# Optimization experiments

Hardware: AMD Instinct MI355X
Metric: run time of the kernel (lower is better)

## Reference

```python
import jax, jax.numpy as jnp
import numpy as np

TR = 14.7e-3
NT = 144
TAU = 1.8
T0 = TAU
T1B = 1.65
FA_PARAMS = (3.0, 12.0)
B = 262144


def _build_buffers():
    # t = arange(Nt)*TR + t0
    t = np.arange(NT, dtype=np.float64) * TR + T0
    # QUADRATIC flip-angle schedule: all t >= t0, so N = Nt
    n = NT
    alpha = FA_PARAMS[0] + (FA_PARAMS[1] - FA_PARAMS[0]) * (np.arange(n) / (n - 1)) ** 2
    # Attenuation recursion: R[0]=1, R[i]=R[i-1]*cos(deg2rad(alpha[i-1])) for t[i]>t0
    R = np.concatenate([[1.0], np.cumprod(np.cos(np.deg2rad(alpha[:-1])))])
    return (t.astype(np.float32), alpha.astype(np.float32), R.astype(np.float32))


def setup_inputs() -> dict:
    key = jax.random.key(0)
    x = jax.random.uniform(key, (B, 4), dtype=jnp.float32)  # [delta_t, s, p, amp]
    t, alpha, R = _build_buffers()
    return {"x": x, "t": jnp.asarray(t), "alpha": jnp.asarray(alpha), "R": jnp.asarray(R)}


def _togammainc(X, A):
    # scipy clamps negatives to 0 in both args, then regularized lower incomplete gamma P(A, X)
    X = jnp.maximum(X, 0.0)
    A = jnp.broadcast_to(jnp.maximum(A, 0.0), X.shape)
    return jax.scipy.special.gammainc(A, X)


def reference(x, t, alpha, R):
    delta_t = x[:, 0:1]  # [B,1]
    s = x[:, 1:2]
    p = x[:, 2:3]
    amp = x[:, 3:4]

    a = 1.0 + p * s                     # [B,1]
    sprime = s + 1.0 / T1B              # [B,1]
    SF = 2.0 * jnp.exp(-delta_t / T1B) * (s / sprime) ** a  # [B,1]

    td = t[None, :] - delta_t           # [B,Nt]
    G = _togammainc(sprime * td, a) - _togammainc(sprime * (td - TAU), a)  # [B,Nt]
    E = jnp.sin(jnp.deg2rad(alpha))     # [Nt]

    S = SF * R[None, :] * G * E[None, :]  # [B,Nt]
    return amp * S
```

## Files before the change

kernel.cpp:

```cpp
#include <hip/hip_runtime.h>
#include <cmath>

#define NT 144

typedef float v2f __attribute__((ext_vector_type(2)));


__global__ __launch_bounds__(256) void dynangio_kernel(
    const float* __restrict__ x,
    const float* __restrict__ t,
    const float* __restrict__ alpha,
    const float* __restrict__ R,
    float* __restrict__ out,
    int B)
{
    __shared__ alignas(16) float sh_t[NT];
    __shared__ alignas(16) float sh_re[NT];
    const int tid = threadIdx.x;
    if (tid < NT) {
        sh_t[tid]  = t[tid];
        sh_re[tid] = R[tid] * sinf(alpha[tid] * 0.017453292519943295f);
    }
    __syncthreads();

    const int c   = tid & 3;
    const int row = blockIdx.x * 64 + (tid >> 2);
    if (row >= B) return;

    const float4 xi = reinterpret_cast<const float4*>(x)[row];
    const float dt  = xi.x;
    const float s   = xi.y;
    const float p   = xi.z;
    const float amp = xi.w;

    const float T1B   = 1.65f;
    const float TAU   = 1.8f;
    const float LOG2E = 1.4426950408889634f;

    const float u  = p * s;
    const float a  = 1.0f + u;
    const float sp = s + (1.0f / T1B);

    float g = 0.035868343f;
    g = g * u - 0.193527818f;
    g = g * u + 0.482199394f;
    g = g * u - 0.756704078f;
    g = g * u + 0.918206857f;
    g = g * u - 0.897056937f;
    g = g * u + 0.988205891f;
    g = g * u - 0.577191652f;
    g = g * u + 1.0f;
    const float Ga1 = (1.0f + u) * g;

    const float d18 = a + 18.0f;
    const float d17 = (a + 17.0f) * d18;
    const float d16 = (a + 16.0f) * d17;
    const float d15 = (a + 15.0f) * d16;
    const float d14 = (a + 14.0f) * d15;
    const float d13 = (a + 13.0f) * d14;
    const float d12 = (a + 12.0f) * d13;
    const float d11 = (a + 11.0f) * d12;
    const float d10 = (a + 10.0f) * d11;
    const float d9  = (a +  9.0f) * d10;
    const float d8  = (a +  8.0f) * d9;
    const float d7  = (a +  7.0f) * d8;
    const float d6  = (a +  6.0f) * d7;
    const float d5  = (a +  5.0f) * d6;
    const float d4  = (a +  4.0f) * d5;
    const float d3  = (a +  3.0f) * d4;
    const float d2  = (a +  2.0f) * d3;
    const float d1  = (a +  1.0f) * d2;

    const float invDG = 1.0f / (d1 * Ga1);

    const float SF = 2.0f * __builtin_amdgcn_exp2f(
        a * (__builtin_amdgcn_logf(s) - __builtin_amdgcn_logf(sp))
        - dt * (LOG2E / T1B));

    const float crow  = amp * SF * invDG;
    const float nspdt = -sp * dt;
    const float spTau = sp * TAU;

    auto elem = [&](float tj, float rej) -> float {
        const float x1 = __builtin_fmaf(sp, tj, nspdt);
        const float x2 = fmaxf(x1 - spTau, 0.0f);
        v2f X; X.x = x1; X.y = x2;
        v2f N = {1.0f, 1.0f};
        N = X*N + d18;  N = X*N + d17;  N = X*N + d16;
        N = X*N + d15;  N = X*N + d14;  N = X*N + d13;
        N = X*N + d12;  N = X*N + d11;  N = X*N + d10;
        N = X*N + d9;   N = X*N + d8;   N = X*N + d7;
        N = X*N + d6;   N = X*N + d5;   N = X*N + d4;
        N = X*N + d3;   N = X*N + d2;   N = X*N + d1;
        v2f L; L.x = __builtin_amdgcn_logf(x1); L.y = __builtin_amdgcn_logf(x2);
        v2f Ee = a * L - X * LOG2E;
        const float e1 = __builtin_amdgcn_exp2f(Ee.x);
        const float e2 = __builtin_amdgcn_exp2f(Ee.y);
        const float gg = __builtin_fmaf(N.x, e1, -(N.y * e2));
        return (crow * rej) * gg;
    };

    float4* __restrict__ orow4 = reinterpret_cast<float4*>(out + (size_t)row * NT);
    const float4* sh_t4  = reinterpret_cast<const float4*>(sh_t);
    const float4* sh_re4 = reinterpret_cast<const float4*>(sh_re);

    #pragma unroll 3
    for (int k = 0; k < 9; ++k) {
        const int ch = c + 4 * k;
        const float4 tj4 = sh_t4[ch];
        const float4 re4 = sh_re4[ch];
        float4 res;
        res.x = elem(tj4.x, re4.x);
        res.y = elem(tj4.y, re4.y);
        res.z = elem(tj4.z, re4.z);
        res.w = elem(tj4.w, re4.w);
        orow4[ch] = res;
    }
}

extern "C" void kernel_launch(void* const* d_in, const int* in_sizes, int n_in,
                              void* d_out, int out_size, void* d_ws, size_t ws_size,
                              hipStream_t stream) {
    const float* x     = (const float*)d_in[0];
    const float* t     = (const float*)d_in[1];
    const float* alpha = (const float*)d_in[2];
    const float* R     = (const float*)d_in[3];
    float* out = (float*)d_out;

    const int B = in_sizes[0] / 4;
    const int rows_per_block = 64;
    const int blocks = (B + rows_per_block - 1) / rows_per_block;
    hipLaunchKernelGGL(dynangio_kernel, dim3(blocks), dim3(256), 0, stream,
                       x, t, alpha, R, out, B);
}
```

Before: 175.0 us.

## Split series polynomial into even/odd Estrin halves and cap occupancy

```diff
diff --git a/kernel.cpp b/kernel.cpp
--- a/kernel.cpp
+++ b/kernel.cpp
@@ -6,7 +6,7 @@
 typedef float v2f __attribute__((ext_vector_type(2)));
 
 
-__global__ __launch_bounds__(256) void dynangio_kernel(
+__global__ __launch_bounds__(256, 4) void dynangio_kernel(
     const float* __restrict__ x,
     const float* __restrict__ t,
     const float* __restrict__ alpha,
@@ -80,40 +80,43 @@
     const float crow  = amp * SF * invDG;
     const float nspdt = -sp * dt;
     const float spTau = sp * TAU;
+    v2f dtv; dtv.x = nspdt; dtv.y = nspdt - spTau;
 
-    auto elem = [&](float tj, float rej) -> float {
-        const float x1 = __builtin_fmaf(sp, tj, nspdt);
-        const float x2 = fmaxf(x1 - spTau, 0.0f);
-        v2f X; X.x = x1; X.y = x2;
-        v2f N = {1.0f, 1.0f};
-        N = X*N + d18;  N = X*N + d17;  N = X*N + d16;
-        N = X*N + d15;  N = X*N + d14;  N = X*N + d13;
-        N = X*N + d12;  N = X*N + d11;  N = X*N + d10;
-        N = X*N + d9;   N = X*N + d8;   N = X*N + d7;
-        N = X*N + d6;   N = X*N + d5;   N = X*N + d4;
-        N = X*N + d3;   N = X*N + d2;   N = X*N + d1;
-        v2f L; L.x = __builtin_amdgcn_logf(x1); L.y = __builtin_amdgcn_logf(x2);
-        v2f Ee = a * L - X * LOG2E;
+    auto elem = [&](float tj, float cr) -> float {
+        v2f tv; tv.x = tj; tv.y = tj;
+        v2f X = sp * tv + dtv;
+        X.y = fmaxf(X.y, 0.0f);
+        const v2f Z = X * X;
+        v2f NE = Z + d17;
+        NE = Z*NE + d15;  NE = Z*NE + d13;  NE = Z*NE + d11;
+        NE = Z*NE + d9;   NE = Z*NE + d7;   NE = Z*NE + d5;
+        NE = Z*NE + d3;   NE = Z*NE + d1;
+        v2f NO = Z*d18 + d16;
+        NO = Z*NO + d14;  NO = Z*NO + d12;  NO = Z*NO + d10;
+        NO = Z*NO + d8;   NO = Z*NO + d6;   NO = Z*NO + d4;
+        NO = Z*NO + d2;
+        const v2f N = X*NO + NE;
+        v2f L; L.x = __builtin_amdgcn_logf(X.x); L.y = __builtin_amdgcn_logf(X.y);
+        const v2f Ee = a * L - X * LOG2E;
         const float e1 = __builtin_amdgcn_exp2f(Ee.x);
         const float e2 = __builtin_amdgcn_exp2f(Ee.y);
-        const float gg = __builtin_fmaf(N.x, e1, -(N.y * e2));
-        return (crow * rej) * gg;
+        return cr * __builtin_fmaf(N.x, e1, -(N.y * e2));
     };
 
     float4* __restrict__ orow4 = reinterpret_cast<float4*>(out + (size_t)row * NT);
     const float4* sh_t4  = reinterpret_cast<const float4*>(sh_t);
     const float4* sh_re4 = reinterpret_cast<const float4*>(sh_re);
 
-    #pragma unroll 3
+    #pragma unroll 1
     for (int k = 0; k < 9; ++k) {
         const int ch = c + 4 * k;
         const float4 tj4 = sh_t4[ch];
         const float4 re4 = sh_re4[ch];
         float4 res;
-        res.x = elem(tj4.x, re4.x);
-        res.y = elem(tj4.y, re4.y);
-        res.z = elem(tj4.z, re4.z);
-        res.w = elem(tj4.w, re4.w);
+        res.x = elem(tj4.x, crow * re4.x);
+        res.y = elem(tj4.y, crow * re4.y);
+        res.z = elem(tj4.z, crow * re4.z);
+        res.w = elem(tj4.w, crow * re4.w);
         orow4[ch] = res;
     }
 }
```

After: 177.1 us. About the same (+1.2%).
